# Kernel optimization log

Hardware: AMD Instinct MI355X
Metric: run time of the kernel (lower is better)

The kernel has to match this reference:

```python
import jax, jax.numpy as jnp
import numpy as np

# MANO fingertip / palm prior vertex indices from contact_loss
_F1 = [697,698,699,700,712,713,714,715,737,738,739,740,741,743,744,745,746,748,749,750,753,754,755,756,757,758,759,760,761,762,763,764,765,766,767,768]
_F2 = [46,47,48,49,164,165,166,167,194,195,223,237,238,280,281,298,301,317,320,323,324,325,326,327,328,329,330,331,332,333,340,341,342,343,344,345,346,347,348,349,350,351,352,353,354,355]
_F3 = [356,357,358,359,375,376,386,387,396,397,402,403,413,429,433,434,435,436,437,438,439,440,441,442,443,444,452,453,454,455,456,459,460,461,462,463,464,465,466,467]
_F4 = [468,469,470,471,484,485,486,496,497,506,507,513,514,524,545,546,547,548,549,550,551,552,553,555,563,564,565,566,567,570,572,573,574,575,576,577,578]
_F5 = [580,581,582,583,600,601,602,614,615,624,625,630,631,641,663,664,665,666,667,668,670,672,680,681,682,683,684,686,687,688,689,690,691,692,693,694,695]
_F0 = [73,96,98,99,772,774,775,777]
PRIOR_IDX = np.array(_F1 + _F2 + _F3 + _F4 + _F5 + _F0, dtype=np.int32)

KL_COEF = 0.005
A_W, B_W, C_W, D_W, E_W = 1.0, 0.1, 1000.0, 10.0, 10.0  # init kwargs a..e


def _nn(src, trg):
    """Brute-force 1-NN: src [B,N1,3] -> trg [B,N2,3].
    Returns (sq_dist [B,N1], idx [B,N1], diff src-near [B,N1,3])."""
    d2 = (jnp.sum(src * src, -1)[:, :, None]
          + jnp.sum(trg * trg, -1)[:, None, :]
          - 2.0 * jnp.einsum('bnd,bmd->bnm', src, trg))  # [B,N1,N2]
    idx = jnp.argmin(d2, axis=-1)
    near = jnp.take_along_axis(trg, idx[:, :, None], axis=1)
    diff = src - near
    return jnp.sum(diff * diff, axis=-1), idx, diff


def _p2p_signed(x, y, x_normals):
    """point2point_signed(x, y, x_normals): signed dist y->x, unsigned x->y."""
    _, yidx, y2x = _nn(y, x)  # nearest x for each y
    y_nn_normal = jnp.take_along_axis(x_normals, yidx[:, :, None], axis=1)
    in_out = jnp.sign(jnp.sum(y_nn_normal * y2x, axis=-1))
    y2x_signed = jnp.sqrt(jnp.sum(y2x * y2x, axis=-1)) * in_out  # [B,P2]
    _, _, x2y = _nn(x, y)  # nearest y for each x
    x2y_dist = jnp.sqrt(jnp.sum(x2y * x2y, axis=-1))  # [B,P1]
    return y2x_signed, x2y_dist


def _forward(recon_xyz, gt_xyz, recon_normals, gt_normals, obj_xyz, mean, log_var, v_weights):
    B = recon_xyz.shape[0]
    f32 = recon_xyz.dtype
    # --- CVAE recon (L2) + KLD ---
    recon_loss = jnp.sum((recon_xyz - gt_xyz) ** 2) / B
    kld = -0.5 * jnp.sum(1.0 + log_var - mean ** 2 - jnp.exp(log_var)) / B * 10.0
    # --- obj -> hand NN (squared dists, pytorch3d knn_points convention) ---
    recon_d2, recon_idx, _ = _nn(obj_xyz, recon_xyz)  # [B,3000]
    gt_d2, _, _ = _nn(obj_xyz, gt_xyz)
    # --- contact map from GT NN dist thresholding ---
    cmap = jnp.sqrt(gt_d2) < 0.005  # [B,3000] bool
    # --- contact_loss: obj NN to prior (fingertip/palm) recon verts ---
    prior = recon_xyz[:, PRIOR_IDX, :]
    obj_cd, _, _ = _nn(obj_xyz, prior)
    n_pts = jnp.sum(cmap.astype(f32))
    contact = 3000.0 * jnp.where(n_pts > 0, jnp.sum(obj_cd * cmap) / (B * n_pts), 0.0)
    # --- CMap_consistency_loss ---
    recon_cmap = jnp.sqrt(recon_d2) < 0.005
    consistency = -5.0 * jnp.sum((recon_cmap & cmap).astype(f32)) / (n_pts + 1e-4)
    # --- inter_penetr_loss: interior obj points via NN-normal dot sign ---
    nn_hand = jnp.take_along_axis(recon_xyz, recon_idx[:, :, None], axis=1)
    nn_normal = jnp.take_along_axis(recon_normals, recon_idx[:, :, None], axis=1)
    interior = jnp.sum((nn_hand - obj_xyz) * nn_normal, axis=-1) > 0
    penetr = 100.0 * jnp.sum(recon_d2 * interior) / B
    # --- loss_cnet: signed chamfer consistency ---
    vw2 = v_weights ** (1.0 / 2.5)
    o2h, h2o = _p2p_signed(recon_xyz, obj_xyz, recon_normals)
    o2h_gt, h2o_gt = _p2p_signed(gt_xyz, obj_xyz, gt_normals)
    w_dist = (o2h_gt < 0.01) & (o2h_gt > -0.005)
    w_neg = o2h < 0.0
    w = jnp.where(w_neg, 1.5, jnp.where(w_dist, 1.0, 0.1))
    loss_h = 35.0 * (1.0 - KL_COEF) * jnp.mean(jnp.abs(jnp.abs(h2o) - jnp.abs(h2o_gt)) * vw2)
    loss_o = 30.0 * (1.0 - KL_COEF) * jnp.mean(jnp.abs(o2h - o2h_gt) * w)
    cnet = loss_h + loss_o
    return (A_W * recon_loss + B_W * kld + C_W * penetr
            + D_W * contact + E_W * consistency + cnet)


def setup_inputs() -> dict:
    key = jax.random.key(0)
    ks = jax.random.split(key, 8)
    B, NH, NO, Z = 32, 778, 3000, 64
    s = 0.05  # meter-scale point clouds so contact thresholds (5mm) are meaningful
    def unit(k, shape):
        v = jax.random.normal(k, shape, dtype=jnp.float32)
        return v / jnp.linalg.norm(v, axis=-1, keepdims=True)
    return {
        'recon_xyz': jax.random.normal(ks[0], (B, NH, 3), dtype=jnp.float32) * s,
        'gt_xyz': jax.random.normal(ks[1], (B, NH, 3), dtype=jnp.float32) * s,
        'recon_normals': unit(ks[2], (B, NH, 3)),
        'gt_normals': unit(ks[3], (B, NH, 3)),
        'obj_xyz': jax.random.normal(ks[4], (B, NO, 3), dtype=jnp.float32) * s,
        'mean': jax.random.normal(ks[5], (B, Z), dtype=jnp.float32),
        'log_var': jax.random.normal(ks[6], (B, Z), dtype=jnp.float32) * 0.1,
        'v_weights': jax.random.uniform(ks[7], (NH,), dtype=jnp.float32),
    }


def reference(recon_xyz, gt_xyz, recon_normals, gt_normals, obj_xyz, mean, log_var, v_weights):
    return _forward(recon_xyz, gt_xyz, recon_normals, gt_normals, obj_xyz, mean, log_var, v_weights)
```

## Files before the change

kernel.cpp:

```cpp
#include <hip/hip_runtime.h>
#include <math.h>


#define NB 32
#define NH 778
#define NO 3000
#define NZ 64
#define NP 204

#define P_OBJ 4
#define OBJ_PTS 1024
#define OBJ_TILES 3
#define JS4 4
#define JC4 195
#define HC12 12
#define HCS12 250

#define NKEY (NB * NO)
#define NHT  (NB * NH)

#define M2_OBJ_BLKS (NB * 47)
#define M2_TAIL_BLKS (NB * NH / 64)
#define M2_BLKS (M2_OBJ_BLKS + M2_TAIL_BLKS)

#define ACCIDX(q, s) ((((q) * 32) + (s)) * 32)
#define ACC_FLOATS (9 * 32 * 32)

typedef unsigned int uint32;

__device__ __constant__ int c_prior[NP] = {
  697,698,699,700,712,713,714,715,737,738,739,740,741,743,744,745,746,748,749,750,
  753,754,755,756,757,758,759,760,761,762,763,764,765,766,767,768,
  46,47,48,49,164,165,166,167,194,195,223,237,238,280,281,298,301,317,320,323,
  324,325,326,327,328,329,330,331,332,333,340,341,342,343,344,345,346,347,348,349,
  350,351,352,353,354,355,
  356,357,358,359,375,376,386,387,396,397,402,403,413,429,433,434,435,436,437,438,
  439,440,441,442,443,444,452,453,454,455,456,459,460,461,462,463,464,465,466,467,
  468,469,470,471,484,485,486,496,497,506,507,513,514,524,545,546,547,548,549,550,
  551,552,553,555,563,564,565,566,567,570,572,573,574,575,576,577,578,
  580,581,582,583,600,601,602,614,615,624,625,630,631,641,663,664,665,666,667,668,
  670,672,680,681,682,683,684,686,687,688,689,690,691,692,693,694,695,
  73,96,98,99,772,774,775,777
};

__device__ __constant__ int c_prior_sorted[NP] = {
  46,47,48,49,73,96,98,99,164,165,166,167,194,
  195,223,237,238,280,281,298,301,317,320,323,324,325,326,327,328,329,330,331,
  332,333,340,341,342,343,344,345,346,347,348,349,350,351,352,353,354,355,356,
  357,358,359,375,376,386,387,
  396,397,402,403,413,429,433,434,435,436,437,438,439,440,441,442,443,444,452,
  453,454,455,456,459,460,461,462,463,464,465,466,467,468,469,470,471,484,485,
  486,496,497,506,507,513,514,524,545,546,547,548,549,550,551,552,553,555,563,
  564,565,566,567,570,572,573,574,575,576,577,578,580,581,582,583,
  600,601,602,614,615,624,625,630,631,641,663,664,665,666,667,668,670,672,680,
  681,682,683,684,686,687,688,689,690,691,692,693,694,695,697,698,699,700,712,
  713,714,715,737,738,739,740,741,743,744,745,746,748,749,750,753,754,755,756,
  757,758,759,760,761,762,763,764,765,766,767,768,772,774,775,777
};
__device__ __constant__ int c_psplit4[5] = {0, 13, 58, 131, 204};

__device__ inline float wave_sum(float v) {
  v += __shfl_down(v, 32);
  v += __shfl_down(v, 16);
  v += __shfl_down(v, 8);
  v += __shfl_down(v, 4);
  v += __shfl_down(v, 2);
  v += __shfl_down(v, 1);
  return v;
}

__device__ __forceinline__ float f_min3(float a, float b, float c) {
  float r;
  asm("v_min3_f32 %0, %1, %2, %3" : "=v"(r) : "v"(a), "v"(b), "v"(c));
  return r;
}
__device__ __forceinline__ float f_packao(float t, int j, uint32 mask) {
  float r;
  asm("v_and_or_b32 %0, %1, %2, %3" : "=v"(r) : "v"(t), "s"(mask), "v"(j));
  return r;
}

__global__ __launch_bounds__(256) void mega1t(
    const float* __restrict__ recon, const float* __restrict__ gt,
    const float* __restrict__ obj,
    float* __restrict__ keyR, float* __restrict__ keyG,
    float* __restrict__ priorK,
    float* __restrict__ minHR, float* __restrict__ minHG,
    float* __restrict__ accs)
{
  const int OBJ_B = NB * OBJ_TILES * JS4;
  const int bid = blockIdx.x;
  const int tid = threadIdx.x;
  const uint32 KMASK = 0xFFFFFC00u;

  if (bid == 0) {
    for (int i = tid; i < ACC_FLOATS; i += 256) accs[i] = 0.0f;
  }

  if (bid < OBJ_B) {
    __shared__ float4 shA[JC4];
    __shared__ float4 shB[JC4];
    const int b     = bid / (OBJ_TILES * JS4);
    const int rem   = bid % (OBJ_TILES * JS4);
    const int tile  = rem / JS4;
    const int split = rem % JS4;
    const int jbase = split * JC4;
    const int jcnt  = (NH - jbase < JC4) ? (NH - jbase) : JC4;

    for (int i = tid; i < jcnt; i += 256) {
      const float* p = recon + ((size_t)b * NH + jbase + i) * 3;
      float x = p[0], y = p[1], z = p[2];
      shA[i] = make_float4(x, y, z, x*x + y*y + z*z);
      const float* q = gt + ((size_t)b * NH + jbase + i) * 3;
      float gx = q[0], gy = q[1], gz = q[2];
      shB[i] = make_float4(gx, gy, gz, gx*gx + gy*gy + gz*gz);
    }
    __syncthreads();

    float nx[P_OBJ], ny[P_OBJ], nz[P_OBJ];
    int ob[P_OBJ]; bool val[P_OBJ];
    #pragma unroll
    for (int m = 0; m < P_OBJ; ++m) {
      int o = tile * OBJ_PTS + m * 256 + tid;
      ob[m] = o; val[m] = (o < NO);
      float x = 0.f, y = 0.f, z = 0.f;
      if (val[m]) {
        const float* op = obj + ((size_t)b * NO + o) * 3;
        x = op[0]; y = op[1]; z = op[2];
      }
      nx[m] = -2.f * x; ny[m] = -2.f * y; nz[m] = -2.f * z;
    }

    float bR[P_OBJ], bG[P_OBJ];
    #pragma unroll
    for (int m = 0; m < P_OBJ; ++m) { bR[m] = 3.4e38f; bG[m] = 3.4e38f; }

#define RSTEP(hh0, hh1, jj0, jj1) \
    { _Pragma("unroll") for (int m = 0; m < P_OBJ; ++m) { \
        float t0 = fmaf(nx[m], hh0.x, hh0.w); t0 = fmaf(ny[m], hh0.y, t0); t0 = fmaf(nz[m], hh0.z, t0); \
        float t1 = fmaf(nx[m], hh1.x, hh1.w); t1 = fmaf(ny[m], hh1.y, t1); t1 = fmaf(nz[m], hh1.z, t1); \
        bR[m] = f_min3(bR[m], f_packao(t0, jj0, KMASK), f_packao(t1, jj1, KMASK)); } }
#define GSTEP(gg0, gg1, jj0, jj1) \
    { _Pragma("unroll") for (int m = 0; m < P_OBJ; ++m) { \
        float u0 = fmaf(nx[m], gg0.x, gg0.w); u0 = fmaf(ny[m], gg0.y, u0); u0 = fmaf(nz[m], gg0.z, u0); \
        float u1 = fmaf(nx[m], gg1.x, gg1.w); u1 = fmaf(ny[m], gg1.y, u1); u1 = fmaf(nz[m], gg1.z, u1); \
        bG[m] = f_min3(bG[m], f_packao(u0, jj0, KMASK), f_packao(u1, jj1, KMASK)); } }

    float4 h0 = shA[0], h1 = shA[1];
    int i = 0;
    for (; i + 3 < jcnt; i += 2) {
      float4 g0 = shB[i], g1 = shB[i + 1];
      RSTEP(h0, h1, jbase + i, jbase + i + 1);
      float4 hn0 = shA[i + 2], hn1 = shA[i + 3];
      GSTEP(g0, g1, jbase + i, jbase + i + 1);
      h0 = hn0; h1 = hn1;
    }
    {
      float4 g0 = shB[i], g1 = shB[i + 1];
      RSTEP(h0, h1, jbase + i, jbase + i + 1);
      GSTEP(g0, g1, jbase + i, jbase + i + 1);
      i += 2;
    }
    for (; i < jcnt; ++i) {
      float4 hh = shA[i], gg = shB[i];
      #pragma unroll
      for (int m = 0; m < P_OBJ; ++m) {
        float t0 = fmaf(nx[m], hh.x, hh.w); t0 = fmaf(ny[m], hh.y, t0); t0 = fmaf(nz[m], hh.z, t0);
        bR[m] = fminf(bR[m], f_packao(t0, jbase + i, KMASK));
        float u0 = fmaf(nx[m], gg.x, gg.w); u0 = fmaf(ny[m], gg.y, u0); u0 = fmaf(nz[m], gg.z, u0);
        bG[m] = fminf(bG[m], f_packao(u0, jbase + i, KMASK));
      }
    }
#undef RSTEP
#undef GSTEP

    float bP[P_OBJ];
    #pragma unroll
    for (int m = 0; m < P_OBJ; ++m) bP[m] = 3.4e38f;
    const int pk0 = c_psplit4[split], pk1 = c_psplit4[split + 1];
    int k = pk0;
    for (; k + 1 < pk1; k += 2) {
      float4 ha = shA[c_prior_sorted[k] - jbase];
      float4 hb = shA[c_prior_sorted[k + 1] - jbase];
      #pragma unroll
      for (int m = 0; m < P_OBJ; ++m) {
        float t = fmaf(nx[m], ha.x, ha.w); t = fmaf(ny[m], ha.y, t); t = fmaf(nz[m], ha.z, t);
        float u = fmaf(nx[m], hb.x, hb.w); u = fmaf(ny[m], hb.y, u); u = fmaf(nz[m], hb.z, u);
        bP[m] = f_min3(bP[m], t, u);
      }
    }
    if (k < pk1) {
      float4 ha = shA[c_prior_sorted[k] - jbase];
      #pragma unroll
      for (int m = 0; m < P_OBJ; ++m) {
        float t = fmaf(nx[m], ha.x, ha.w); t = fmaf(ny[m], ha.y, t); t = fmaf(nz[m], ha.z, t);
        bP[m] = fminf(bP[m], t);
      }
    }

    #pragma unroll
    for (int m = 0; m < P_OBJ; ++m) {
      if (!val[m]) continue;
      const size_t idx = (size_t)split * NKEY + (size_t)b * NO + ob[m];
      keyR[idx] = bR[m];
      keyG[idx] = bG[m];
      priorK[idx] = bP[m];
    }
  } else {
    __shared__ float4 sO[HCS12];
    const int bid2 = bid - OBJ_B;
    const int oc = bid2 % HC12;
    const int b  = bid2 / HC12;

    const float* Ob = obj + ((size_t)b * NO + oc * HCS12) * 3;
    for (int i2 = tid; i2 < HCS12; i2 += 256) {
      float x = Ob[3*i2], y = Ob[3*i2+1], z = Ob[3*i2+2];
      sO[i2] = make_float4(x, y, z, x*x + y*y + z*z);
    }
    __syncthreads();

    float nrx[3], nry[3], nrz[3];
    float ngx[3], ngy[3], ngz[3];
    #pragma unroll
    for (int m = 0; m < 3; ++m) {
      const int j = m * 256 + tid;
      const float* rp = recon + ((size_t)b * NH + j) * 3;
      const float* gp = gt    + ((size_t)b * NH + j) * 3;
      nrx[m] = -2.f*rp[0]; nry[m] = -2.f*rp[1]; nrz[m] = -2.f*rp[2];
      ngx[m] = -2.f*gp[0]; ngy[m] = -2.f*gp[1]; ngz[m] = -2.f*gp[2];
    }

    float mR[3], mG[3];
    #pragma unroll
    for (int m = 0; m < 3; ++m) { mR[m] = 3.4e38f; mG[m] = 3.4e38f; }

#define HSTEP(oo0, oo1) \
    { _Pragma("unroll") for (int m = 0; m < 3; ++m) { \
        float t0 = fmaf(nrx[m], oo0.x, oo0.w); t0 = fmaf(nry[m], oo0.y, t0); t0 = fmaf(nrz[m], oo0.z, t0); \
        float t1 = fmaf(nrx[m], oo1.x, oo1.w); t1 = fmaf(nry[m], oo1.y, t1); t1 = fmaf(nrz[m], oo1.z, t1); \
        mR[m] = f_min3(mR[m], t0, t1); \
        float u0 = fmaf(ngx[m], oo0.x, oo0.w); u0 = fmaf(ngy[m], oo0.y, u0); u0 = fmaf(ngz[m], oo0.z, u0); \
        float u1 = fmaf(ngx[m], oo1.x, oo1.w); u1 = fmaf(ngy[m], oo1.y, u1); u1 = fmaf(ngz[m], oo1.z, u1); \
        mG[m] = f_min3(mG[m], u0, u1); } }

    float4 o0 = sO[0], o1 = sO[1];
    int k2 = 0;
    for (; k2 + 3 < HCS12; k2 += 2) {
      float4 a0 = sO[k2 + 2], a1 = sO[k2 + 3];
      HSTEP(o0, o1);
      o0 = a0; o1 = a1;
    }
    HSTEP(o0, o1);
    k2 += 2;
    for (; k2 < HCS12; ++k2) {
      float4 oc4 = sO[k2];
      #pragma unroll
      for (int m = 0; m < 3; ++m) {
        float t0 = fmaf(nrx[m], oc4.x, oc4.w); t0 = fmaf(nry[m], oc4.y, t0); t0 = fmaf(nrz[m], oc4.z, t0);
        mR[m] = fminf(mR[m], t0);
        float u0 = fmaf(ngx[m], oc4.x, oc4.w); u0 = fmaf(ngy[m], oc4.y, u0); u0 = fmaf(ngz[m], oc4.z, u0);
        mG[m] = fminf(mG[m], u0);
      }
    }
#undef HSTEP

    #pragma unroll
    for (int m = 0; m < 3; ++m) {
      const int j = m * 256 + tid;
      const size_t idx = (size_t)oc * NHT + (size_t)b * NH + j;
      minHR[idx] = mR[m];
      minHG[idx] = mG[m];
    }

    const int tw = bid2 & 3;
    if ((tid >> 6) == tw) {
      const int j3 = 768 + (tid & 63);
      const bool v3 = (j3 < NH);
      float rx=0.f,ry=0.f,rz=0.f,gx=0.f,gy=0.f,gz=0.f;
      if (v3) {
        const float* rp = recon + ((size_t)b * NH + j3) * 3;
        const float* gp = gt    + ((size_t)b * NH + j3) * 3;
        rx=rp[0];ry=rp[1];rz=rp[2]; gx=gp[0];gy=gp[1];gz=gp[2];
      }
      const float n3rx=-2.f*rx, n3ry=-2.f*ry, n3rz=-2.f*rz;
      const float n3gx=-2.f*gx, n3gy=-2.f*gy, n3gz=-2.f*gz;
      float m3R = 3.4e38f, m3G = 3.4e38f;
      int k3 = 0;
      for (; k3 + 1 < HCS12; k3 += 2) {
        float4 q0 = sO[k3], q1 = sO[k3 + 1];
        float t0 = fmaf(n3rx, q0.x, q0.w); t0 = fmaf(n3ry, q0.y, t0); t0 = fmaf(n3rz, q0.z, t0);
        float t1 = fmaf(n3rx, q1.x, q1.w); t1 = fmaf(n3ry, q1.y, t1); t1 = fmaf(n3rz, q1.z, t1);
        m3R = f_min3(m3R, t0, t1);
        float u0 = fmaf(n3gx, q0.x, q0.w); u0 = fmaf(n3gy, q0.y, u0); u0 = fmaf(n3gz, q0.z, u0);
        float u1 = fmaf(n3gx, q1.x, q1.w); u1 = fmaf(n3gy, q1.y, u1); u1 = fmaf(n3gz, q1.z, u1);
        m3G = f_min3(m3G, u0, u1);
      }
      if (HCS12 & 1) {
        float4 q0 = sO[HCS12 - 1];
        float t0 = fmaf(n3rx, q0.x, q0.w); t0 = fmaf(n3ry, q0.y, t0); t0 = fmaf(n3rz, q0.z, t0);
        m3R = fminf(m3R, t0);
        float u0 = fmaf(n3gx, q0.x, q0.w); u0 = fmaf(n3gy, q0.y, u0); u0 = fmaf(n3gz, q0.z, u0);
        m3G = fminf(m3G, u0);
      }
      if (v3) {
        const size_t idx = (size_t)oc * NHT + (size_t)b * NH + j3;
        minHR[idx] = m3R;
        minHG[idx] = m3G;
      }
    }
  }
}

__global__ __launch_bounds__(64) void mega2s(
    const float* __restrict__ recon, const float* __restrict__ gt,
    const float* __restrict__ rnorm, const float* __restrict__ gnorm,
    const float* __restrict__ obj,
    const float* __restrict__ mean, const float* __restrict__ logv,
    const float* __restrict__ vw,
    const float* __restrict__ keyR, const float* __restrict__ keyG,
    const float* __restrict__ priorK,
    const float* __restrict__ minHR, const float* __restrict__ minHG,
    float* __restrict__ accs)
{
  const int bid = blockIdx.x;
  const int tid = threadIdx.x;
  const int line = bid & 31;

  if (bid < M2_OBJ_BLKS) {
    const int b = bid / 47;
    const int o = (bid % 47) * 64 + tid;
    float penetr = 0.f, nptsv = 0.f, contactv = 0.f, consistv = 0.f, lossov = 0.f;
    if (o < NO) {
      const float* op = obj + ((size_t)b * NO + o) * 3;
      const float ox = op[0], oy = op[1], oz = op[2];
      const float o2 = ox*ox + oy*oy + oz*oz;
      const size_t base = (size_t)b * NO + o;

      float kR = 3.4e38f, kG = 3.4e38f, bP = 3.4e38f;
      #pragma unroll
      for (int s = 0; s < JS4; ++s) {
        kR = fminf(kR, keyR[(size_t)s * NKEY + base]);
        kG = fminf(kG, keyG[(size_t)s * NKEY + base]);
        bP = fminf(bP, priorK[(size_t)s * NKEY + base]);
      }
      uint32 kRb = __float_as_uint(kR), kGb = __float_as_uint(kG);
      int idxR = (int)(kRb & 0x3FFu), idxG = (int)(kGb & 0x3FFu);
      float d2R = fmaxf(__uint_as_float(kRb & 0xFFFFFC00u) + o2, 0.f);
      float d2G = fmaxf(__uint_as_float(kGb & 0xFFFFFC00u) + o2, 0.f);
      float d2P = fmaxf(bP + o2, 0.f);

      const float* hR = recon + ((size_t)b * NH + idxR) * 3;
      const float* nR = rnorm + ((size_t)b * NH + idxR) * 3;
      float dotR = (ox - hR[0]) * nR[0] + (oy - hR[1]) * nR[1] + (oz - hR[2]) * nR[2];
      const float* hG = gt + ((size_t)b * NH + idxG) * 3;
      const float* nG = gnorm + ((size_t)b * NH + idxG) * 3;
      float dotG = (ox - hG[0]) * nG[0] + (oy - hG[1]) * nG[1] + (oz - hG[2]) * nG[2];

      float sgnR = (dotR > 0.f) ? 1.f : ((dotR < 0.f) ? -1.f : 0.f);
      float sgnG = (dotG > 0.f) ? 1.f : ((dotG < 0.f) ? -1.f : 0.f);
      float sR_ = sqrtf(d2R), sG_ = sqrtf(d2G);
      float o2h = sR_ * sgnR, o2hg = sG_ * sgnG;

      bool interior = dotR < 0.f;
      bool cmap = sG_ < 0.005f;
      bool rcmap = sR_ < 0.005f;

      penetr   = interior ? d2R : 0.f;
      nptsv    = cmap ? 1.f : 0.f;
      contactv = cmap ? d2P : 0.f;
      consistv = (cmap && rcmap) ? 1.f : 0.f;
      float w = (o2h < 0.f) ? 1.5f
              : (((o2hg < 0.01f) && (o2hg > -0.005f)) ? 1.f : 0.1f);
      lossov = fabsf(o2h - o2hg) * w;
    }

    float vals[5] = {penetr, nptsv, contactv, consistv, lossov};
    #pragma unroll
    for (int q = 0; q < 5; ++q) {
      float s = wave_sum(vals[q]);
      if (tid == 0) atomicAdd(&accs[ACCIDX(q, line)], s);
    }
  } else {
    const int t = (bid - M2_OBJ_BLKS) * 64 + tid;
    float lossh = 0.f, rsum = 0.f, ksum = 0.f;
    {
      const float* rp = recon + (size_t)t * 3;
      const float* gp = gt + (size_t)t * 3;
      float rx = rp[0], ry = rp[1], rz = rp[2];
      float gx = gp[0], gy = gp[1], gz = gp[2];
      float d0 = rx - gx, d1 = ry - gy, d2 = rz - gz;
      rsum = d0*d0 + d1*d1 + d2*d2;

      float mRt = 3.4e38f, mGt = 3.4e38f;
      #pragma unroll
      for (int c = 0; c < HC12; ++c) {
        mRt = fminf(mRt, minHR[(size_t)c * NHT + t]);
        mGt = fminf(mGt, minHG[(size_t)c * NHT + t]);
      }
      float r2 = rx*rx + ry*ry + rz*rz;
      float g2 = gx*gx + gy*gy + gz*gz;
      float d2Rh = fmaxf(mRt + r2, 0.f);
      float d2Gh = fmaxf(mGt + g2, 0.f);
      int j = t % NH;
      lossh = fabsf(sqrtf(d2Rh) - sqrtf(d2Gh)) * powf(vw[j], 0.4f);
    }
    if (t < NB * NZ) {
      float m = mean[t], lv = logv[t];
      ksum = 1.f + lv - m * m - expf(lv);
    }
    float vals[3] = {lossh, rsum, ksum};
    #pragma unroll
    for (int q = 0; q < 3; ++q) {
      float s = wave_sum(vals[q]);
      if (tid == 0) atomicAdd(&accs[ACCIDX(5 + q, line)], s);
    }
  }
}

__global__ void final_fb(const float* __restrict__ a, float* __restrict__ out) {
  __shared__ float sums[8];
  const int q = threadIdx.x;
  if (q < 8) {
    float s = 0.f;
    for (int l = 0; l < 32; ++l) s += a[ACCIDX(q, l)];
    sums[q] = s;
  }
  __syncthreads();
  if (threadIdx.x == 0) {
    const float recon_loss = sums[6] / (float)NB;
    const float kld = -0.5f * sums[7] / (float)NB * 10.f;
    const float penetr = 100.f * sums[0] / (float)NB;
    const float npts = sums[1];
    const float contact = (npts > 0.f) ? (3000.f * sums[2] / ((float)NB * npts)) : 0.f;
    const float consistency = -5.f * sums[3] / (npts + 0.0001f);
    const float lossh = 35.f * (1.f - 0.005f) * (sums[5] / (float)(NB * NH));
    const float losso = 30.f * (1.f - 0.005f) * (sums[4] / (float)(NB * NO));
    out[0] = recon_loss + 0.1f * kld + 1000.f * penetr + 10.f * contact
           + 10.f * consistency + lossh + losso;
  }
}

__global__ __launch_bounds__(256) void obj_mono(
    const float* __restrict__ recon, const float* __restrict__ gt,
    const float* __restrict__ rnorm, const float* __restrict__ gnorm,
    const float* __restrict__ obj, float* __restrict__ accs)
{
  __shared__ float4 sR[NH];
  __shared__ float4 sG[NH];
  __shared__ float red[4][5];
  const int b = blockIdx.x / 12;
  const int tile = blockIdx.x % 12;
  const int tid = threadIdx.x;
  for (int i = tid; i < NH; i += 256) {
    const float* p = recon + ((size_t)b * NH + i) * 3;
    float x = p[0], y = p[1], z = p[2];
    sR[i] = make_float4(x, y, z, x*x + y*y + z*z);
    const float* q = gt + ((size_t)b * NH + i) * 3;
    float gx = q[0], gy = q[1], gz = q[2];
    sG[i] = make_float4(gx, gy, gz, gx*gx + gy*gy + gz*gz);
  }
  __syncthreads();
  const int o = tile * 256 + tid;
  float penetr = 0.f, nptsv = 0.f, contactv = 0.f, consistv = 0.f, lossov = 0.f;
  if (o < NO) {
    const float* op = obj + ((size_t)b * NO + o) * 3;
    const float ox = op[0], oy = op[1], oz = op[2];
    const float nx = -2.f*ox, ny = -2.f*oy, nz = -2.f*oz;
    const float o2 = ox*ox + oy*oy + oz*oz;
    float bR = 3.4e38f, bG = 3.4e38f; int iR = 0, iG = 0;
    for (int i = 0; i < NH; ++i) {
      float4 h = sR[i];
      float t = fmaf(nx, h.x, h.w); t = fmaf(ny, h.y, t); t = fmaf(nz, h.z, t);
      if (t < bR) { bR = t; iR = i; }
      float4 g = sG[i];
      float u = fmaf(nx, g.x, g.w); u = fmaf(ny, g.y, u); u = fmaf(nz, g.z, u);
      if (u < bG) { bG = u; iG = i; }
    }
    float bP = 3.4e38f;
    for (int k = 0; k < NP; ++k) {
      float4 h = sR[c_prior[k]];
      float t = fmaf(nx, h.x, h.w); t = fmaf(ny, h.y, t); t = fmaf(nz, h.z, t);
      bP = fminf(bP, t);
    }
    float d2R = fmaxf(bR + o2, 0.f);
    float d2G = fmaxf(bG + o2, 0.f);
    float d2P = fmaxf(bP + o2, 0.f);
    float4 hR = sR[iR];
    const float* nR = rnorm + ((size_t)b * NH + iR) * 3;
    float dotR = (ox-hR.x)*nR[0] + (oy-hR.y)*nR[1] + (oz-hR.z)*nR[2];
    float4 hG = sG[iG];
    const float* nG = gnorm + ((size_t)b * NH + iG) * 3;
    float dotG = (ox-hG.x)*nG[0] + (oy-hG.y)*nG[1] + (oz-hG.z)*nG[2];
    float sgnR = (dotR > 0.f) ? 1.f : ((dotR < 0.f) ? -1.f : 0.f);
    float sgnG = (dotG > 0.f) ? 1.f : ((dotG < 0.f) ? -1.f : 0.f);
    float sR_ = sqrtf(d2R), sG_ = sqrtf(d2G);
    float o2h = sR_*sgnR, o2hg = sG_*sgnG;
    bool interior = dotR < 0.f;
    bool cmap = sG_ < 0.005f, rcmap = sR_ < 0.005f;
    penetr = interior ? d2R : 0.f;
    nptsv = cmap ? 1.f : 0.f;
    contactv = cmap ? d2P : 0.f;
    consistv = (cmap && rcmap) ? 1.f : 0.f;
    float w = (o2h < 0.f) ? 1.5f : (((o2hg < 0.01f) && (o2hg > -0.005f)) ? 1.f : 0.1f);
    lossov = fabsf(o2h - o2hg) * w;
  }
  float vals[5] = {penetr, nptsv, contactv, consistv, lossov};
  const int lane = tid & 63, wv = tid >> 6;
  for (int q = 0; q < 5; ++q) {
    float s = wave_sum(vals[q]);
    if (lane == 0) red[wv][q] = s;
  }
  __syncthreads();
  if (tid < 5) {
    float s = red[0][tid] + red[1][tid] + red[2][tid] + red[3][tid];
    atomicAdd(&accs[ACCIDX(tid, blockIdx.x & 31)], s);
  }
}

__global__ __launch_bounds__(256) void hand_full(
    const float* __restrict__ recon, const float* __restrict__ gt,
    const float* __restrict__ obj, const float* __restrict__ vw,
    float* __restrict__ accs)
{
  __shared__ float4 sO[500];
  __shared__ float red[4];
  const int b = blockIdx.x >> 2;
  const int j = ((blockIdx.x & 3) << 8) + threadIdx.x;
  const bool valid = j < NH;
  float rx=0,ry=0,rz=0,gx=0,gy=0,gz=0;
  if (valid) {
    const float* rp = recon + ((size_t)b * NH + j) * 3;
    const float* gp = gt + ((size_t)b * NH + j) * 3;
    rx=rp[0];ry=rp[1];rz=rp[2]; gx=gp[0];gy=gp[1];gz=gp[2];
  }
  const float nrx=-2.f*rx, nry=-2.f*ry, nrz=-2.f*rz;
  const float ngx=-2.f*gx, ngy=-2.f*gy, ngz=-2.f*gz;
  const float r2 = rx*rx+ry*ry+rz*rz, g2 = gx*gx+gy*gy+gz*gz;
  float mR = 3.4e38f, mG = 3.4e38f;
  for (int oc = 0; oc < 6; ++oc) {
    __syncthreads();
    const float* Ob = obj + ((size_t)b * NO + oc * 500) * 3;
    for (int i = threadIdx.x; i < 500; i += 256) {
      float x = Ob[3*i], y = Ob[3*i+1], z = Ob[3*i+2];
      sO[i] = make_float4(x, y, z, x*x + y*y + z*z);
    }
    __syncthreads();
    if (valid) {
      for (int k = 0; k < 500; ++k) {
        float4 o4 = sO[k];
        float t = fmaf(nrx,o4.x,o4.w); t = fmaf(nry,o4.y,t); t = fmaf(nrz,o4.z,t);
        mR = fminf(mR, t);
        float u = fmaf(ngx,o4.x,o4.w); u = fmaf(ngy,o4.y,u); u = fmaf(ngz,o4.z,u);
        mG = fminf(mG, u);
      }
    }
  }
  float lossh = valid ? fabsf(sqrtf(fmaxf(mR+r2,0.f)) - sqrtf(fmaxf(mG+g2,0.f))) * powf(vw[j], 0.4f) : 0.f;
  const int lane = threadIdx.x & 63, wv = threadIdx.x >> 6;
  float s = wave_sum(lossh);
  if (lane == 0) red[wv] = s;
  __syncthreads();
  if (threadIdx.x == 0) atomicAdd(&accs[ACCIDX(5, blockIdx.x & 31)], red[0]+red[1]+red[2]+red[3]);
}

__global__ __launch_bounds__(256) void tail_nomins(
    const float* __restrict__ recon, const float* __restrict__ gt,
    const float* __restrict__ mean, const float* __restrict__ logv,
    float* __restrict__ accs)
{
  __shared__ float red[4][2];
  const int t = blockIdx.x * 256 + threadIdx.x;
  float rsum = 0.f, ksum = 0.f;
  if (t < NB * NH) {
    const float* rp = recon + (size_t)t * 3;
    const float* gp = gt + (size_t)t * 3;
    float d0 = rp[0]-gp[0], d1 = rp[1]-gp[1], d2 = rp[2]-gp[2];
    rsum = d0*d0 + d1*d1 + d2*d2;
  }
  if (t < NB * NZ) {
    float m = mean[t], lv = logv[t];
    ksum = 1.f + lv - m*m - expf(lv);
  }
  float vals[2] = {rsum, ksum};
  const int lane = threadIdx.x & 63, wv = threadIdx.x >> 6;
  for (int q = 0; q < 2; ++q) {
    float s = wave_sum(vals[q]);
    if (lane == 0) red[wv][q] = s;
  }
  __syncthreads();
  if (threadIdx.x < 2) {
    float s = red[0][threadIdx.x] + red[1][threadIdx.x] + red[2][threadIdx.x] + red[3][threadIdx.x];
    atomicAdd(&accs[ACCIDX(6 + threadIdx.x, blockIdx.x & 31)], s);
  }
}

__global__ void init_small(float* accs) {
  for (int i = threadIdx.x; i < ACC_FLOATS; i += 256) accs[i] = 0.0f;
}

extern "C" void kernel_launch(void* const* d_in, const int* in_sizes, int n_in,
                              void* d_out, int out_size, void* d_ws, size_t ws_size,
                              hipStream_t stream) {
  const float* recon = (const float*)d_in[0];
  const float* gt    = (const float*)d_in[1];
  const float* rnorm = (const float*)d_in[2];
  const float* gnorm = (const float*)d_in[3];
  const float* obj   = (const float*)d_in[4];
  const float* mean  = (const float*)d_in[5];
  const float* logv  = (const float*)d_in[6];
  const float* vw    = (const float*)d_in[7];
  float* out = (float*)d_out;

  float* accs = (float*)d_ws;
  float* base = (float*)((char*)d_ws + ACC_FLOATS * sizeof(float));

  const size_t needed = ACC_FLOATS * sizeof(float)
                      + (3ull * JS4 * NKEY + 2ull * HC12 * NHT) * sizeof(float);

  if (ws_size >= needed) {
    float* keyR   = base;
    float* keyG   = keyR + (size_t)JS4 * NKEY;
    float* priorK = keyG + (size_t)JS4 * NKEY;
    float* minHR  = priorK + (size_t)JS4 * NKEY;
    float* minHG  = minHR + (size_t)HC12 * NHT;
    const int g1 = NB * OBJ_TILES * JS4 + NB * HC12;
    mega1t<<<g1, 256, 0, stream>>>(
        recon, gt, obj, keyR, keyG, priorK, minHR, minHG, accs);
    mega2s<<<M2_BLKS, 64, 0, stream>>>(
        recon, gt, rnorm, gnorm, obj, mean, logv, vw,
        keyR, keyG, priorK, minHR, minHG, accs);
    final_fb<<<1, 64, 0, stream>>>(accs, out);
  } else {
    init_small<<<1, 256, 0, stream>>>(accs);
    obj_mono<<<NB * 12, 256, 0, stream>>>(recon, gt, rnorm, gnorm, obj, accs);
    hand_full<<<NB * 4, 256, 0, stream>>>(recon, gt, obj, vw, accs);
    tail_nomins<<<(NB * NH + 255) / 256, 256, 0, stream>>>(recon, gt, mean, logv, accs);
    final_fb<<<1, 64, 0, stream>>>(accs, out);
  }
}
```

Measured before the change: 108.7 us.

## Split first-stage kernel into single-wavefront blocks with finer object and hand tiling

Shrinks the first-stage kernel from 256-thread to 64-thread blocks. Object points are re-tiled into 12 tiles of 256 per batch, and the hand-side work is split into two j-tiles with six points per thread, which raises the block count and balances the load across CUs. The tail hand points (768..777) are now computed by only 10 rotated lanes in the jt==0 blocks instead of a whole wavefront. Accumulator zeroing is spread over 8 blocks. The trade is more blocks that each reload shared tiles, and more register pressure from PH=6 in the hand path.

```diff
diff --git a/kernel.cpp b/kernel.cpp
--- a/kernel.cpp
+++ b/kernel.cpp
@@ -9,12 +9,17 @@
 #define NP 204
 
 #define P_OBJ 4
-#define OBJ_PTS 1024
-#define OBJ_TILES 3
+#define OTIL 12
 #define JS4 4
 #define JC4 195
 #define HC12 12
 #define HCS12 250
+#define PH 6
+#define JT2 2
+
+#define OBJ_B (NB * OTIL * JS4)
+#define HAND_B (NB * JT2 * HC12)
+#define M1_BLKS (OBJ_B + HAND_B)
 
 #define NKEY (NB * NO)
 #define NHT  (NB * NH)
@@ -80,7 +85,7 @@
   return r;
 }
 
-__global__ __launch_bounds__(256) void mega1t(
+__global__ __launch_bounds__(64) void mega1w(
     const float* __restrict__ recon, const float* __restrict__ gt,
     const float* __restrict__ obj,
     float* __restrict__ keyR, float* __restrict__ keyG,
@@ -88,26 +93,26 @@
     float* __restrict__ minHR, float* __restrict__ minHG,
     float* __restrict__ accs)
 {
-  const int OBJ_B = NB * OBJ_TILES * JS4;
   const int bid = blockIdx.x;
   const int tid = threadIdx.x;
   const uint32 KMASK = 0xFFFFFC00u;
 
-  if (bid == 0) {
-    for (int i = tid; i < ACC_FLOATS; i += 256) accs[i] = 0.0f;
+  if (bid < 8) {
+    const int base0 = bid * (ACC_FLOATS / 8);
+    for (int i = tid; i < ACC_FLOATS / 8; i += 64) accs[base0 + i] = 0.0f;
   }
 
   if (bid < OBJ_B) {
     __shared__ float4 shA[JC4];
     __shared__ float4 shB[JC4];
-    const int b     = bid / (OBJ_TILES * JS4);
-    const int rem   = bid % (OBJ_TILES * JS4);
+    const int b     = bid / (OTIL * JS4);
+    const int rem   = bid % (OTIL * JS4);
     const int tile  = rem / JS4;
     const int split = rem % JS4;
     const int jbase = split * JC4;
     const int jcnt  = (NH - jbase < JC4) ? (NH - jbase) : JC4;
 
-    for (int i = tid; i < jcnt; i += 256) {
+    for (int i = tid; i < jcnt; i += 64) {
       const float* p = recon + ((size_t)b * NH + jbase + i) * 3;
       float x = p[0], y = p[1], z = p[2];
       shA[i] = make_float4(x, y, z, x*x + y*y + z*z);
@@ -121,7 +126,7 @@
     int ob[P_OBJ]; bool val[P_OBJ];
     #pragma unroll
     for (int m = 0; m < P_OBJ; ++m) {
-      int o = tile * OBJ_PTS + m * 256 + tid;
+      int o = tile * 256 + m * 64 + tid;
       ob[m] = o; val[m] = (o < NO);
       float x = 0.f, y = 0.f, z = 0.f;
       if (val[m]) {
@@ -209,33 +214,35 @@
   } else {
     __shared__ float4 sO[HCS12];
     const int bid2 = bid - OBJ_B;
-    const int oc = bid2 % HC12;
-    const int b  = bid2 / HC12;
+    const int b   = bid2 / (JT2 * HC12);
+    const int rem = bid2 % (JT2 * HC12);
+    const int jt  = rem / HC12;
+    const int oc  = rem % HC12;
 
     const float* Ob = obj + ((size_t)b * NO + oc * HCS12) * 3;
-    for (int i2 = tid; i2 < HCS12; i2 += 256) {
+    for (int i2 = tid; i2 < HCS12; i2 += 64) {
       float x = Ob[3*i2], y = Ob[3*i2+1], z = Ob[3*i2+2];
       sO[i2] = make_float4(x, y, z, x*x + y*y + z*z);
     }
     __syncthreads();
 
-    float nrx[3], nry[3], nrz[3];
-    float ngx[3], ngy[3], ngz[3];
-    #pragma unroll
-    for (int m = 0; m < 3; ++m) {
-      const int j = m * 256 + tid;
+    float nrx[PH], nry[PH], nrz[PH];
+    float ngx[PH], ngy[PH], ngz[PH];
+    #pragma unroll
+    for (int m = 0; m < PH; ++m) {
+      const int j = jt * 384 + m * 64 + tid;
       const float* rp = recon + ((size_t)b * NH + j) * 3;
       const float* gp = gt    + ((size_t)b * NH + j) * 3;
       nrx[m] = -2.f*rp[0]; nry[m] = -2.f*rp[1]; nrz[m] = -2.f*rp[2];
       ngx[m] = -2.f*gp[0]; ngy[m] = -2.f*gp[1]; ngz[m] = -2.f*gp[2];
     }
 
-    float mR[3], mG[3];
-    #pragma unroll
-    for (int m = 0; m < 3; ++m) { mR[m] = 3.4e38f; mG[m] = 3.4e38f; }
+    float mR[PH], mG[PH];
+    #pragma unroll
+    for (int m = 0; m < PH; ++m) { mR[m] = 3.4e38f; mG[m] = 3.4e38f; }
 
 #define HSTEP(oo0, oo1) \
-    { _Pragma("unroll") for (int m = 0; m < 3; ++m) { \
+    { _Pragma("unroll") for (int m = 0; m < PH; ++m) { \
         float t0 = fmaf(nrx[m], oo0.x, oo0.w); t0 = fmaf(nry[m], oo0.y, t0); t0 = fmaf(nrz[m], oo0.z, t0); \
         float t1 = fmaf(nrx[m], oo1.x, oo1.w); t1 = fmaf(nry[m], oo1.y, t1); t1 = fmaf(nrz[m], oo1.z, t1); \
         mR[m] = f_min3(mR[m], t0, t1); \
@@ -251,58 +258,34 @@
       o0 = a0; o1 = a1;
     }
     HSTEP(o0, o1);
-    k2 += 2;
-    for (; k2 < HCS12; ++k2) {
-      float4 oc4 = sO[k2];
-      #pragma unroll
-      for (int m = 0; m < 3; ++m) {
-        float t0 = fmaf(nrx[m], oc4.x, oc4.w); t0 = fmaf(nry[m], oc4.y, t0); t0 = fmaf(nrz[m], oc4.z, t0);
-        mR[m] = fminf(mR[m], t0);
-        float u0 = fmaf(ngx[m], oc4.x, oc4.w); u0 = fmaf(ngy[m], oc4.y, u0); u0 = fmaf(ngz[m], oc4.z, u0);
-        mG[m] = fminf(mG[m], u0);
-      }
-    }
 #undef HSTEP
 
     #pragma unroll
-    for (int m = 0; m < 3; ++m) {
-      const int j = m * 256 + tid;
+    for (int m = 0; m < PH; ++m) {
+      const int j = jt * 384 + m * 64 + tid;
       const size_t idx = (size_t)oc * NHT + (size_t)b * NH + j;
       minHR[idx] = mR[m];
       minHG[idx] = mG[m];
     }
 
-    const int tw = bid2 & 3;
-    if ((tid >> 6) == tw) {
-      const int j3 = 768 + (tid & 63);
-      const bool v3 = (j3 < NH);
-      float rx=0.f,ry=0.f,rz=0.f,gx=0.f,gy=0.f,gz=0.f;
-      if (v3) {
+    if (jt == 0) {
+      const int r = (tid + oc * 5) & 63;
+      if (r < 10) {
+        const int j3 = 768 + r;
         const float* rp = recon + ((size_t)b * NH + j3) * 3;
         const float* gp = gt    + ((size_t)b * NH + j3) * 3;
-        rx=rp[0];ry=rp[1];rz=rp[2]; gx=gp[0];gy=gp[1];gz=gp[2];
-      }
-      const float n3rx=-2.f*rx, n3ry=-2.f*ry, n3rz=-2.f*rz;
-      const float n3gx=-2.f*gx, n3gy=-2.f*gy, n3gz=-2.f*gz;
-      float m3R = 3.4e38f, m3G = 3.4e38f;
-      int k3 = 0;
-      for (; k3 + 1 < HCS12; k3 += 2) {
-        float4 q0 = sO[k3], q1 = sO[k3 + 1];
-        float t0 = fmaf(n3rx, q0.x, q0.w); t0 = fmaf(n3ry, q0.y, t0); t0 = fmaf(n3rz, q0.z, t0);
-        float t1 = fmaf(n3rx, q1.x, q1.w); t1 = fmaf(n3ry, q1.y, t1); t1 = fmaf(n3rz, q1.z, t1);
-        m3R = f_min3(m3R, t0, t1);
-        float u0 = fmaf(n3gx, q0.x, q0.w); u0 = fmaf(n3gy, q0.y, u0); u0 = fmaf(n3gz, q0.z, u0);
-        float u1 = fmaf(n3gx, q1.x, q1.w); u1 = fmaf(n3gy, q1.y, u1); u1 = fmaf(n3gz, q1.z, u1);
-        m3G = f_min3(m3G, u0, u1);
-      }
-      if (HCS12 & 1) {
-        float4 q0 = sO[HCS12 - 1];
-        float t0 = fmaf(n3rx, q0.x, q0.w); t0 = fmaf(n3ry, q0.y, t0); t0 = fmaf(n3rz, q0.z, t0);
-        m3R = fminf(m3R, t0);
-        float u0 = fmaf(n3gx, q0.x, q0.w); u0 = fmaf(n3gy, q0.y, u0); u0 = fmaf(n3gz, q0.z, u0);
-        m3G = fminf(m3G, u0);
-      }
-      if (v3) {
+        const float n3rx=-2.f*rp[0], n3ry=-2.f*rp[1], n3rz=-2.f*rp[2];
+        const float n3gx=-2.f*gp[0], n3gy=-2.f*gp[1], n3gz=-2.f*gp[2];
+        float m3R = 3.4e38f, m3G = 3.4e38f;
+        for (int k3 = 0; k3 + 1 < HCS12; k3 += 2) {
+          float4 q0 = sO[k3], q1 = sO[k3 + 1];
+          float t0 = fmaf(n3rx, q0.x, q0.w); t0 = fmaf(n3ry, q0.y, t0); t0 = fmaf(n3rz, q0.z, t0);
+          float t1 = fmaf(n3rx, q1.x, q1.w); t1 = fmaf(n3ry, q1.y, t1); t1 = fmaf(n3rz, q1.z, t1);
+          m3R = f_min3(m3R, t0, t1);
+          float u0 = fmaf(n3gx, q0.x, q0.w); u0 = fmaf(n3gy, q0.y, u0); u0 = fmaf(n3gz, q0.z, u0);
+          float u1 = fmaf(n3gx, q1.x, q1.w); u1 = fmaf(n3gy, q1.y, u1); u1 = fmaf(n3gz, q1.z, u1);
+          m3G = f_min3(m3G, u0, u1);
+        }
         const size_t idx = (size_t)oc * NHT + (size_t)b * NH + j3;
         minHR[idx] = m3R;
         minHG[idx] = m3G;
@@ -623,8 +606,7 @@
     float* priorK = keyG + (size_t)JS4 * NKEY;
     float* minHR  = priorK + (size_t)JS4 * NKEY;
     float* minHG  = minHR + (size_t)HC12 * NHT;
-    const int g1 = NB * OBJ_TILES * JS4 + NB * HC12;
-    mega1t<<<g1, 256, 0, stream>>>(
+    mega1w<<<M1_BLKS, 64, 0, stream>>>(
         recon, gt, obj, keyR, keyG, priorK, minHR, minHG, accs);
     mega2s<<<M2_BLKS, 64, 0, stream>>>(
         recon, gt, rnorm, gnorm, obj, mean, logv, vw,
```

New measurement: 123.9 us. +14.0%, slower.

## Precompute float4 point arrays in prep kernel and read them directly from global memory

Applied to the files above, without the earlier changes.

A new prep kernel converts recon, gt and object points into float4 arrays holding xyz and the squared norm, and also zeroes the accumulators. The main distance kernel then drops its shared-memory staging and __syncthreads, reading the uniform float4 operands straight from global memory, which should hit in cache. This removes the per-block staging cost and the barrier, but adds a kernel launch and an extra pass through global memory. The inner-loop loads become wave-uniform global or scalar loads instead of LDS reads, which may have higher latency.

```diff
diff --git a/kernel.cpp b/kernel.cpp
--- a/kernel.cpp
+++ b/kernel.cpp
@@ -80,26 +80,42 @@
   return r;
 }
 
-__global__ __launch_bounds__(256) void mega1t(
+__global__ __launch_bounds__(256) void prep(
     const float* __restrict__ recon, const float* __restrict__ gt,
     const float* __restrict__ obj,
+    float4* __restrict__ recon4, float4* __restrict__ gt4,
+    float4* __restrict__ obj4, float* __restrict__ accs)
+{
+  const int t = blockIdx.x * 256 + threadIdx.x;
+  if (t < ACC_FLOATS) accs[t] = 0.0f;
+  if (t < NHT) {
+    const float* p = recon + (size_t)t * 3;
+    float x = p[0], y = p[1], z = p[2];
+    recon4[t] = make_float4(x, y, z, x*x + y*y + z*z);
+    const float* q = gt + (size_t)t * 3;
+    float gx = q[0], gy = q[1], gz = q[2];
+    gt4[t] = make_float4(gx, gy, gz, gx*gx + gy*gy + gz*gz);
+  }
+  if (t < NKEY) {
+    const float* o = obj + (size_t)t * 3;
+    float x = o[0], y = o[1], z = o[2];
+    obj4[t] = make_float4(x, y, z, x*x + y*y + z*z);
+  }
+}
+
+__global__ __launch_bounds__(256) void mega1g(
+    const float4* __restrict__ recon4, const float4* __restrict__ gt4,
+    const float4* __restrict__ obj4,
     float* __restrict__ keyR, float* __restrict__ keyG,
     float* __restrict__ priorK,
-    float* __restrict__ minHR, float* __restrict__ minHG,
-    float* __restrict__ accs)
+    float* __restrict__ minHR, float* __restrict__ minHG)
 {
   const int OBJ_B = NB * OBJ_TILES * JS4;
   const int bid = blockIdx.x;
   const int tid = threadIdx.x;
   const uint32 KMASK = 0xFFFFFC00u;
 
-  if (bid == 0) {
-    for (int i = tid; i < ACC_FLOATS; i += 256) accs[i] = 0.0f;
-  }
-
   if (bid < OBJ_B) {
-    __shared__ float4 shA[JC4];
-    __shared__ float4 shB[JC4];
     const int b     = bid / (OBJ_TILES * JS4);
     const int rem   = bid % (OBJ_TILES * JS4);
     const int tile  = rem / JS4;
@@ -107,15 +123,9 @@
     const int jbase = split * JC4;
     const int jcnt  = (NH - jbase < JC4) ? (NH - jbase) : JC4;
 
-    for (int i = tid; i < jcnt; i += 256) {
-      const float* p = recon + ((size_t)b * NH + jbase + i) * 3;
-      float x = p[0], y = p[1], z = p[2];
-      shA[i] = make_float4(x, y, z, x*x + y*y + z*z);
-      const float* q = gt + ((size_t)b * NH + jbase + i) * 3;
-      float gx = q[0], gy = q[1], gz = q[2];
-      shB[i] = make_float4(gx, gy, gz, gx*gx + gy*gy + gz*gz);
-    }
-    __syncthreads();
+    const float4* __restrict__ A  = recon4 + (size_t)b * NH + jbase;
+    const float4* __restrict__ Bq = gt4    + (size_t)b * NH + jbase;
+    const float4* __restrict__ A0 = recon4 + (size_t)b * NH;
 
     float nx[P_OBJ], ny[P_OBJ], nz[P_OBJ];
     int ob[P_OBJ]; bool val[P_OBJ];
@@ -125,8 +135,8 @@
       ob[m] = o; val[m] = (o < NO);
       float x = 0.f, y = 0.f, z = 0.f;
       if (val[m]) {
-        const float* op = obj + ((size_t)b * NO + o) * 3;
-        x = op[0]; y = op[1]; z = op[2];
+        float4 ov = obj4[(size_t)b * NO + o];
+        x = ov.x; y = ov.y; z = ov.z;
       }
       nx[m] = -2.f * x; ny[m] = -2.f * y; nz[m] = -2.f * z;
     }
@@ -146,23 +156,23 @@
         float u1 = fmaf(nx[m], gg1.x, gg1.w); u1 = fmaf(ny[m], gg1.y, u1); u1 = fmaf(nz[m], gg1.z, u1); \
         bG[m] = f_min3(bG[m], f_packao(u0, jj0, KMASK), f_packao(u1, jj1, KMASK)); } }
 
-    float4 h0 = shA[0], h1 = shA[1];
+    float4 h0 = A[0], h1 = A[1];
     int i = 0;
     for (; i + 3 < jcnt; i += 2) {
-      float4 g0 = shB[i], g1 = shB[i + 1];
+      float4 g0 = Bq[i], g1 = Bq[i + 1];
       RSTEP(h0, h1, jbase + i, jbase + i + 1);
-      float4 hn0 = shA[i + 2], hn1 = shA[i + 3];
+      float4 hn0 = A[i + 2], hn1 = A[i + 3];
       GSTEP(g0, g1, jbase + i, jbase + i + 1);
       h0 = hn0; h1 = hn1;
     }
     {
-      float4 g0 = shB[i], g1 = shB[i + 1];
+      float4 g0 = Bq[i], g1 = Bq[i + 1];
       RSTEP(h0, h1, jbase + i, jbase + i + 1);
       GSTEP(g0, g1, jbase + i, jbase + i + 1);
       i += 2;
     }
     for (; i < jcnt; ++i) {
-      float4 hh = shA[i], gg = shB[i];
+      float4 hh = A[i], gg = Bq[i];
       #pragma unroll
       for (int m = 0; m < P_OBJ; ++m) {
         float t0 = fmaf(nx[m], hh.x, hh.w); t0 = fmaf(ny[m], hh.y, t0); t0 = fmaf(nz[m], hh.z, t0);
@@ -180,8 +190,8 @@
     const int pk0 = c_psplit4[split], pk1 = c_psplit4[split + 1];
     int k = pk0;
     for (; k + 1 < pk1; k += 2) {
-      float4 ha = shA[c_prior_sorted[k] - jbase];
-      float4 hb = shA[c_prior_sorted[k + 1] - jbase];
+      float4 ha = A0[c_prior_sorted[k]];
+      float4 hb = A0[c_prior_sorted[k + 1]];
       #pragma unroll
       for (int m = 0; m < P_OBJ; ++m) {
         float t = fmaf(nx[m], ha.x, ha.w); t = fmaf(ny[m], ha.y, t); t = fmaf(nz[m], ha.z, t);
@@ -190,7 +200,7 @@
       }
     }
     if (k < pk1) {
-      float4 ha = shA[c_prior_sorted[k] - jbase];
+      float4 ha = A0[c_prior_sorted[k]];
       #pragma unroll
       for (int m = 0; m < P_OBJ; ++m) {
         float t = fmaf(nx[m], ha.x, ha.w); t = fmaf(ny[m], ha.y, t); t = fmaf(nz[m], ha.z, t);
@@ -207,27 +217,21 @@
       priorK[idx] = bP[m];
     }
   } else {
-    __shared__ float4 sO[HCS12];
     const int bid2 = bid - OBJ_B;
     const int oc = bid2 % HC12;
     const int b  = bid2 / HC12;
 
-    const float* Ob = obj + ((size_t)b * NO + oc * HCS12) * 3;
-    for (int i2 = tid; i2 < HCS12; i2 += 256) {
-      float x = Ob[3*i2], y = Ob[3*i2+1], z = Ob[3*i2+2];
-      sO[i2] = make_float4(x, y, z, x*x + y*y + z*z);
-    }
-    __syncthreads();
+    const float4* __restrict__ O4 = obj4 + (size_t)b * NO + oc * HCS12;
 
     float nrx[3], nry[3], nrz[3];
     float ngx[3], ngy[3], ngz[3];
     #pragma unroll
     for (int m = 0; m < 3; ++m) {
       const int j = m * 256 + tid;
-      const float* rp = recon + ((size_t)b * NH + j) * 3;
-      const float* gp = gt    + ((size_t)b * NH + j) * 3;
-      nrx[m] = -2.f*rp[0]; nry[m] = -2.f*rp[1]; nrz[m] = -2.f*rp[2];
-      ngx[m] = -2.f*gp[0]; ngy[m] = -2.f*gp[1]; ngz[m] = -2.f*gp[2];
+      float4 rv = recon4[(size_t)b * NH + j];
+      float4 gv = gt4[(size_t)b * NH + j];
+      nrx[m] = -2.f*rv.x; nry[m] = -2.f*rv.y; nrz[m] = -2.f*rv.z;
+      ngx[m] = -2.f*gv.x; ngy[m] = -2.f*gv.y; ngz[m] = -2.f*gv.z;
     }
 
     float mR[3], mG[3];
@@ -243,25 +247,14 @@
         float u1 = fmaf(ngx[m], oo1.x, oo1.w); u1 = fmaf(ngy[m], oo1.y, u1); u1 = fmaf(ngz[m], oo1.z, u1); \
         mG[m] = f_min3(mG[m], u0, u1); } }
 
-    float4 o0 = sO[0], o1 = sO[1];
+    float4 o0 = O4[0], o1 = O4[1];
     int k2 = 0;
     for (; k2 + 3 < HCS12; k2 += 2) {
-      float4 a0 = sO[k2 + 2], a1 = sO[k2 + 3];
+      float4 a0 = O4[k2 + 2], a1 = O4[k2 + 3];
       HSTEP(o0, o1);
       o0 = a0; o1 = a1;
     }
     HSTEP(o0, o1);
-    k2 += 2;
-    for (; k2 < HCS12; ++k2) {
-      float4 oc4 = sO[k2];
-      #pragma unroll
-      for (int m = 0; m < 3; ++m) {
-        float t0 = fmaf(nrx[m], oc4.x, oc4.w); t0 = fmaf(nry[m], oc4.y, t0); t0 = fmaf(nrz[m], oc4.z, t0);
-        mR[m] = fminf(mR[m], t0);
-        float u0 = fmaf(ngx[m], oc4.x, oc4.w); u0 = fmaf(ngy[m], oc4.y, u0); u0 = fmaf(ngz[m], oc4.z, u0);
-        mG[m] = fminf(mG[m], u0);
-      }
-    }
 #undef HSTEP
 
     #pragma unroll
@@ -276,31 +269,22 @@
     if ((tid >> 6) == tw) {
       const int j3 = 768 + (tid & 63);
       const bool v3 = (j3 < NH);
-      float rx=0.f,ry=0.f,rz=0.f,gx=0.f,gy=0.f,gz=0.f;
+      float n3rx=0.f,n3ry=0.f,n3rz=0.f,n3gx=0.f,n3gy=0.f,n3gz=0.f;
       if (v3) {
-        const float* rp = recon + ((size_t)b * NH + j3) * 3;
-        const float* gp = gt    + ((size_t)b * NH + j3) * 3;
-        rx=rp[0];ry=rp[1];rz=rp[2]; gx=gp[0];gy=gp[1];gz=gp[2];
-      }
-      const float n3rx=-2.f*rx, n3ry=-2.f*ry, n3rz=-2.f*rz;
-      const float n3gx=-2.f*gx, n3gy=-2.f*gy, n3gz=-2.f*gz;
+        float4 rv = recon4[(size_t)b * NH + j3];
+        float4 gv = gt4[(size_t)b * NH + j3];
+        n3rx=-2.f*rv.x; n3ry=-2.f*rv.y; n3rz=-2.f*rv.z;
+        n3gx=-2.f*gv.x; n3gy=-2.f*gv.y; n3gz=-2.f*gv.z;
+      }
       float m3R = 3.4e38f, m3G = 3.4e38f;
-      int k3 = 0;
-      for (; k3 + 1 < HCS12; k3 += 2) {
-        float4 q0 = sO[k3], q1 = sO[k3 + 1];
+      for (int k3 = 0; k3 + 1 < HCS12; k3 += 2) {
+        float4 q0 = O4[k3], q1 = O4[k3 + 1];
         float t0 = fmaf(n3rx, q0.x, q0.w); t0 = fmaf(n3ry, q0.y, t0); t0 = fmaf(n3rz, q0.z, t0);
         float t1 = fmaf(n3rx, q1.x, q1.w); t1 = fmaf(n3ry, q1.y, t1); t1 = fmaf(n3rz, q1.z, t1);
         m3R = f_min3(m3R, t0, t1);
         float u0 = fmaf(n3gx, q0.x, q0.w); u0 = fmaf(n3gy, q0.y, u0); u0 = fmaf(n3gz, q0.z, u0);
         float u1 = fmaf(n3gx, q1.x, q1.w); u1 = fmaf(n3gy, q1.y, u1); u1 = fmaf(n3gz, q1.z, u1);
         m3G = f_min3(m3G, u0, u1);
-      }
-      if (HCS12 & 1) {
-        float4 q0 = sO[HCS12 - 1];
-        float t0 = fmaf(n3rx, q0.x, q0.w); t0 = fmaf(n3ry, q0.y, t0); t0 = fmaf(n3rz, q0.z, t0);
-        m3R = fminf(m3R, t0);
-        float u0 = fmaf(n3gx, q0.x, q0.w); u0 = fmaf(n3gy, q0.y, u0); u0 = fmaf(n3gz, q0.z, u0);
-        m3G = fminf(m3G, u0);
       }
       if (v3) {
         const size_t idx = (size_t)oc * NHT + (size_t)b * NH + j3;
@@ -614,8 +598,10 @@
   float* accs = (float*)d_ws;
   float* base = (float*)((char*)d_ws + ACC_FLOATS * sizeof(float));
 
+  const size_t slice_floats = 3ull * JS4 * NKEY + 2ull * HC12 * NHT;
   const size_t needed = ACC_FLOATS * sizeof(float)
-                      + (3ull * JS4 * NKEY + 2ull * HC12 * NHT) * sizeof(float);
+                      + slice_floats * sizeof(float)
+                      + (2ull * NHT + NKEY) * sizeof(float4);
 
   if (ws_size >= needed) {
     float* keyR   = base;
@@ -623,9 +609,15 @@
     float* priorK = keyG + (size_t)JS4 * NKEY;
     float* minHR  = priorK + (size_t)JS4 * NKEY;
     float* minHG  = minHR + (size_t)HC12 * NHT;
+    float4* recon4 = (float4*)(minHG + (size_t)HC12 * NHT);
+    float4* gt4    = recon4 + NHT;
+    float4* obj4   = gt4 + NHT;
+
+    prep<<<(NKEY + 255) / 256, 256, 0, stream>>>(
+        recon, gt, obj, recon4, gt4, obj4, accs);
     const int g1 = NB * OBJ_TILES * JS4 + NB * HC12;
-    mega1t<<<g1, 256, 0, stream>>>(
-        recon, gt, obj, keyR, keyG, priorK, minHR, minHG, accs);
+    mega1g<<<g1, 256, 0, stream>>>(
+        recon4, gt4, obj4, keyR, keyG, priorK, minHR, minHG);
     mega2s<<<M2_BLKS, 64, 0, stream>>>(
         recon, gt, rnorm, gnorm, obj, mean, logv, vw,
         keyR, keyG, priorK, minHR, minHG, accs);
```

Result: slower. 133.9 us (+23.1%).
